# Kernel optimization log

Measured on AMD Instinct MI355X. Metric: run time of the kernel, lower is better.

## Reference

```python
import jax, jax.numpy as jnp
import numpy as np

B, N, D, F = 32, 96, 32, 16


def setup_inputs() -> dict:
    key = jax.random.key(0)
    ks = jax.random.split(key, 10)
    s = 0.1
    nodes = jax.random.normal(ks[0], (B, N, D), dtype=jnp.float32)
    edges = jax.random.normal(ks[1], (B, N * N, F), dtype=jnp.float32)
    mask = (jax.random.uniform(ks[2], (B, N * N, 1)) < 0.3).astype(jnp.float32)
    # GRU_Aggregator: Linear(F -> D*D) + ReLU
    W_agg = jax.random.normal(ks[3], (F, D * D), dtype=jnp.float32) * s
    b_agg = jax.random.normal(ks[4], (D * D,), dtype=jnp.float32) * s
    # GRU_Combiner: nn.GRU(input_size=D, hidden_size=D), gate order r,z,n
    w_ih = jax.random.normal(ks[5], (3 * D, D), dtype=jnp.float32) * s
    w_hh = jax.random.normal(ks[6], (3 * D, D), dtype=jnp.float32) * s
    b_ih = jax.random.normal(ks[7], (3 * D,), dtype=jnp.float32) * s
    b_hh = jax.random.normal(ks[8], (3 * D,), dtype=jnp.float32) * s
    return {"nodes": nodes, "edges": edges, "mask": mask,
            "W_agg": W_agg, "b_agg": b_agg,
            "w_ih": w_ih, "w_hh": w_hh, "b_ih": b_ih, "b_hh": b_hh}


def _gru_cell(h, x, w_ih, w_hh, b_ih, b_hh):
    # torch nn.GRU cell: gates in (r, z, n) order
    gi = x @ w_ih.T + b_ih  # [..., 3D]
    gh = h @ w_hh.T + b_hh
    i_r, i_z, i_n = jnp.split(gi, 3, axis=-1)
    h_r, h_z, h_n = jnp.split(gh, 3, axis=-1)
    r = jax.nn.sigmoid(i_r + h_r)
    z = jax.nn.sigmoid(i_z + h_z)
    n = jnp.tanh(i_n + r * h_n)
    return (1.0 - z) * n + z * h


def reference(nodes, edges, mask, W_agg, b_agg, w_ih, w_hh, b_ih, b_hh):
    b, n, d = nodes.shape
    # edge-conditioned per-edge matrices A: [B, N*N, D, D]
    A = jax.nn.relu(edges @ W_agg + b_agg).reshape(b, n * n, d, d)
    # state_j = nodes.repeat(1, N, 1): entry (i*N + j) is nodes[:, j]
    state_j = jnp.tile(nodes, (1, n, 1))  # [B, N*N, D]
    messages = jnp.einsum('bepq,beq->bep', A, state_j)  # [B, N*N, D]
    masked = (messages * mask).reshape(b, n, n, d)
    agg_m = masked.sum(axis=2)  # [B, N, D]
    # GRU combiner: sequence [old_state, agg_messages], h0 = 0, take last output
    h = jnp.zeros((b, n, d), dtype=nodes.dtype)
    h = _gru_cell(h, nodes, w_ih, w_hh, b_ih, b_hh)
    h = _gru_cell(h, agg_m, w_ih, w_hh, b_ih, b_hh)
    return h
```

## Files before the change

kernel.cpp:

```cpp
#include <hip/hip_runtime.h>
#include <math.h>

#define BB 32
#define NN 96
#define DD 32
#define FF 16
#define NE (NN * NN)
#define PAIRS (BB * NN)
#define PPB 6
#define GRID_F (PAIRS / PPB)
#define EG 6

__device__ __forceinline__ float dot32(const float* __restrict__ x,
                                       const float* __restrict__ w) {
    float s = 0.f;
    #pragma unroll
    for (int u = 0; u < 8; ++u) {
        float4 a = *(const float4*)(x + 4 * u);
        float4 c = *(const float4*)(w + 4 * u);
        s = fmaf(a.x, c.x, fmaf(a.y, c.y, fmaf(a.z, c.z, fmaf(a.w, c.w, s))));
    }
    return s;
}
__device__ __forceinline__ float sigm(float x) { return 1.f / (1.f + expf(-x)); }

__global__ __launch_bounds__(512, 2)
void mp_fused(const float* __restrict__ nodes, const float* __restrict__ edges,
              const float* __restrict__ mask, const float* __restrict__ W_agg,
              const float* __restrict__ b_agg,
              const float* __restrict__ w_ih, const float* __restrict__ w_hh,
              const float* __restrict__ b_ih, const float* __restrict__ b_hh,
              float* __restrict__ out) {
    __shared__ __align__(16) float Wl[FF * 1024];
    __shared__ __align__(16) float nodl[NN * DD];
    __shared__ int jlist[2][NN];
    __shared__ int jcnt[2];
    __shared__ __align__(16) float aggv[PPB][DD];
    __shared__ __align__(16) float h1v[PPB][DD];
    __shared__ float bih_s[96], bhh_s[96];

    const int tid  = threadIdx.x;
    const int lane = tid & 63;
    const int wv   = tid >> 6;
    const int tq   = wv & 3;
    const int psel = wv >> 2;
    const int pair0 = blockIdx.x * PPB;
    const int b  = pair0 / NN;
    const int i0 = pair0 % NN;
    const int l8 = lane & 7;
    const int lp = lane >> 3;
    const int wbase = 256 * tq + 4 * lane;

    for (int v = tid; v < 4096; v += 512)
        ((float4*)Wl)[v] = ((const float4*)W_agg)[v];
    for (int v = tid; v < 768; v += 512)
        ((float4*)nodl)[v] = ((const float4*)(nodes + b * NN * DD))[v];

    const float4 bvv = *(const float4*)(b_agg + wbase);

    for (int pr = 0; pr < 3; ++pr) {
        __syncthreads();
        if (tid < 2) jcnt[tid] = 0;
        __syncthreads();
        if (tid < 2 * NN) {
            const int ps = tid / NN, col = tid % NN;
            const int ii = i0 + 2 * pr + ps;
            if (mask[(size_t)b * NE + (size_t)ii * NN + col] != 0.f) {
                int p = atomicAdd(&jcnt[ps], 1);
                jlist[ps][p] = col;
            }
        }
        __syncthreads();
        const int i = i0 + 2 * pr + psel;
        const int cnt = __builtin_amdgcn_readfirstlane(jcnt[psel]);
        const float4* ebase4 =
            (const float4*)(edges + ((size_t)b * NE + (size_t)i * NN) * FF);

        float aggacc = 0.f;
        for (int e0 = 0; e0 < cnt; e0 += EG) {
            int jj[EG];
            #pragma unroll
            for (int e = 0; e < EG; ++e) {
                int idx = e0 + e; if (idx > cnt - 1) idx = cnt - 1;
                jj[e] = __builtin_amdgcn_readfirstlane(jlist[psel][idx]);
            }
            float acc[EG][4];
            #pragma unroll
            for (int e = 0; e < EG; ++e) {
                acc[e][0] = bvv.x; acc[e][1] = bvv.y;
                acc[e][2] = bvv.z; acc[e][3] = bvv.w;
            }
            #pragma unroll
            for (int u = 0; u < 4; ++u) {
                float4 ev[EG];
                #pragma unroll
                for (int e = 0; e < EG; ++e) ev[e] = ebase4[jj[e] * 4 + u];
                #pragma unroll
                for (int f2 = 0; f2 < 4; ++f2) {
                    const float4 w4 =
                        *(const float4*)(Wl + (4 * u + f2) * 1024 + wbase);
                    #pragma unroll
                    for (int e = 0; e < EG; ++e) {
                        const float ef = (f2 == 0) ? ev[e].x : (f2 == 1) ? ev[e].y
                                       : (f2 == 2) ? ev[e].z : ev[e].w;
                        acc[e][0] = fmaf(ef, w4.x, acc[e][0]);
                        acc[e][1] = fmaf(ef, w4.y, acc[e][1]);
                        acc[e][2] = fmaf(ef, w4.z, acc[e][2]);
                        acc[e][3] = fmaf(ef, w4.w, acc[e][3]);
                    }
                }
            }
            #pragma unroll
            for (int e = 0; e < EG; ++e) {
                if (e0 + e < cnt) {
                    const float4 x4 =
                        *(const float4*)(nodl + jj[e] * DD + 4 * l8);
                    aggacc = fmaf(fmaxf(acc[e][0], 0.f), x4.x, aggacc);
                    aggacc = fmaf(fmaxf(acc[e][1], 0.f), x4.y, aggacc);
                    aggacc = fmaf(fmaxf(acc[e][2], 0.f), x4.z, aggacc);
                    aggacc = fmaf(fmaxf(acc[e][3], 0.f), x4.w, aggacc);
                }
            }
        }
        aggacc += __shfl_xor(aggacc, 1, 64);
        aggacc += __shfl_xor(aggacc, 2, 64);
        aggacc += __shfl_xor(aggacc, 4, 64);
        if (l8 == 0) aggv[2 * pr + psel][8 * tq + lp] = aggacc;
    }

    __syncthreads();
    float* wihL = Wl;
    float* whhL = Wl + 3456;
    for (int v = tid; v < 768; v += 512) {
        int row = v >> 3, c4 = v & 7;
        *(float4*)&wihL[row * 36 + c4 * 4] = ((const float4*)w_ih)[v];
        *(float4*)&whhL[row * 36 + c4 * 4] = ((const float4*)w_hh)[v];
    }
    if (tid < 96) { bih_s[tid] = b_ih[tid]; bhh_s[tid] = b_hh[tid]; }
    __syncthreads();

    if (tid < PPB * DD) {
        const int pp = tid >> 5, d = tid & 31;
        const float* x = nodl + (i0 + pp) * DD;
        float gi_r = dot32(x, &wihL[(0 * 32 + d) * 36]) + bih_s[d];
        float gi_z = dot32(x, &wihL[(1 * 32 + d) * 36]) + bih_s[32 + d];
        float gi_n = dot32(x, &wihL[(2 * 32 + d) * 36]) + bih_s[64 + d];
        float r1 = sigm(gi_r + bhh_s[d]);
        float z1 = sigm(gi_z + bhh_s[32 + d]);
        float n1 = tanhf(gi_n + r1 * bhh_s[64 + d]);
        h1v[pp][d] = (1.f - z1) * n1;
    }
    __syncthreads();
    if (tid < PPB * DD) {
        const int pp = tid >> 5, d = tid & 31;
        const float* a  = &aggv[pp][0];
        const float* h1 = &h1v[pp][0];
        float gi_r = dot32(a, &wihL[(0 * 32 + d) * 36]) + bih_s[d];
        float gi_z = dot32(a, &wihL[(1 * 32 + d) * 36]) + bih_s[32 + d];
        float gi_n = dot32(a, &wihL[(2 * 32 + d) * 36]) + bih_s[64 + d];
        float gh_r = dot32(h1, &whhL[(0 * 32 + d) * 36]) + bhh_s[d];
        float gh_z = dot32(h1, &whhL[(1 * 32 + d) * 36]) + bhh_s[32 + d];
        float gh_n = dot32(h1, &whhL[(2 * 32 + d) * 36]) + bhh_s[64 + d];
        float r2 = sigm(gi_r + gh_r);
        float z2 = sigm(gi_z + gh_z);
        float n2 = tanhf(gi_n + r2 * gh_n);
        float h2 = (1.f - z2) * n2 + z2 * h1[d];
        out[(size_t)(pair0 + pp) * DD + d] = h2;
    }
}

extern "C" void kernel_launch(void* const* d_in, const int* in_sizes, int n_in,
                              void* d_out, int out_size, void* d_ws, size_t ws_size,
                              hipStream_t stream) {
    const float* nodes = (const float*)d_in[0];
    const float* edges = (const float*)d_in[1];
    const float* mask  = (const float*)d_in[2];
    const float* W_agg = (const float*)d_in[3];
    const float* b_agg = (const float*)d_in[4];
    const float* w_ih  = (const float*)d_in[5];
    const float* w_hh  = (const float*)d_in[6];
    const float* b_ih  = (const float*)d_in[7];
    const float* b_hh  = (const float*)d_in[8];
    float* out = (float*)d_out;

    mp_fused<<<GRID_F, 512, 0, stream>>>(nodes, edges, mask, W_agg, b_agg,
                                         w_ih, w_hh, b_ih, b_hh, out);
}
```

Baseline: 158.0 us.

## Gather masked edges into LDS and load-balance edge groups across waves

Doubles the rows per block to 12 and the block size to 1024 threads. All masked edge rows for those 12 rows are gathered into shared memory in one coalesced pass before any compute starts. Work is then split into a flat list of six-edge groups that the four wave slots take in turn, with partial results merged through shared-memory atomics. This replaces the old per-row-pair sequential passes and their barriers, and it spreads uneven mask counts across waves. The cost is more shared memory, at most one block per CU, and half as many blocks in the grid.

After: 311.9 us. 97.5% more time.

```diff
diff --git a/kernel.cpp b/kernel.cpp
--- a/kernel.cpp
+++ b/kernel.cpp
@@ -7,9 +7,10 @@
 #define FF 16
 #define NE (NN * NN)
 #define PAIRS (BB * NN)
-#define PPB 6
+#define PPB 12
 #define GRID_F (PAIRS / PPB)
 #define EG 6
+#define MAXG (PPB * 16)
 
 __device__ __forceinline__ float dot32(const float* __restrict__ x,
                                        const float* __restrict__ w) {
@@ -24,7 +25,7 @@
 }
 __device__ __forceinline__ float sigm(float x) { return 1.f / (1.f + expf(-x)); }
 
-__global__ __launch_bounds__(512, 2)
+__global__ __launch_bounds__(1024)
 void mp_fused(const float* __restrict__ nodes, const float* __restrict__ edges,
               const float* __restrict__ mask, const float* __restrict__ W_agg,
               const float* __restrict__ b_agg,
@@ -33,17 +34,21 @@
               float* __restrict__ out) {
     __shared__ __align__(16) float Wl[FF * 1024];
     __shared__ __align__(16) float nodl[NN * DD];
-    __shared__ int jlist[2][NN];
-    __shared__ int jcnt[2];
-    __shared__ __align__(16) float aggv[PPB][DD];
-    __shared__ __align__(16) float h1v[PPB][DD];
+    __shared__ float4 ebufq[PPB * 384];
+    __shared__ int   jlf[PPB * NN];
+    __shared__ int   jcnt[PPB];
+    __shared__ int   g2p[MAXG];
+    __shared__ int   g2e0[MAXG];
+    __shared__ int   gtot_s;
+    __shared__ float aggv[PPB][DD];
+    __shared__ float h1v[PPB][DD];
     __shared__ float bih_s[96], bhh_s[96];
 
     const int tid  = threadIdx.x;
     const int lane = tid & 63;
     const int wv   = tid >> 6;
     const int tq   = wv & 3;
-    const int psel = wv >> 2;
+    const int s    = wv >> 2;
     const int pair0 = blockIdx.x * PPB;
     const int b  = pair0 / NN;
     const int i0 = pair0 % NN;
@@ -51,90 +56,124 @@
     const int lp = lane >> 3;
     const int wbase = 256 * tq + 4 * lane;
 
-    for (int v = tid; v < 4096; v += 512)
-        ((float4*)Wl)[v] = ((const float4*)W_agg)[v];
-    for (int v = tid; v < 768; v += 512)
-        ((float4*)nodl)[v] = ((const float4*)(nodes + b * NN * DD))[v];
-
+    if (tid < PPB) jcnt[tid] = 0;
+    if (tid < PPB * DD) ((float*)aggv)[tid] = 0.f;
+    #pragma unroll
+    for (int c = 0; c < 4; ++c)
+        ((float4*)Wl)[c * 1024 + tid] = ((const float4*)W_agg)[c * 1024 + tid];
+    if (tid < 768)
+        ((float4*)nodl)[tid] = ((const float4*)(nodes + b * NN * DD))[tid];
     const float4 bvv = *(const float4*)(b_agg + wbase);
-
-    for (int pr = 0; pr < 3; ++pr) {
-        __syncthreads();
-        if (tid < 2) jcnt[tid] = 0;
-        __syncthreads();
-        if (tid < 2 * NN) {
-            const int ps = tid / NN, col = tid % NN;
-            const int ii = i0 + 2 * pr + ps;
-            if (mask[(size_t)b * NE + (size_t)ii * NN + col] != 0.f) {
-                int p = atomicAdd(&jcnt[ps], 1);
-                jlist[ps][p] = col;
-            }
-        }
-        __syncthreads();
-        const int i = i0 + 2 * pr + psel;
-        const int cnt = __builtin_amdgcn_readfirstlane(jcnt[psel]);
-        const float4* ebase4 =
-            (const float4*)(edges + ((size_t)b * NE + (size_t)i * NN) * FF);
-
-        float aggacc = 0.f;
-        for (int e0 = 0; e0 < cnt; e0 += EG) {
-            int jj[EG];
+    __syncthreads();
+
+    for (int v = tid; v < PPB * NN; v += 1024) {
+        const int p = v / NN, col = v % NN;
+        if (mask[(size_t)b * NE + (size_t)(i0 + p) * NN + col] != 0.f) {
+            int pos = atomicAdd(&jcnt[p], 1);
+            jlf[p * NN + pos] = col;
+        }
+    }
+    __syncthreads();
+
+    if (tid < PPB) {
+        int gs = 0;
+        for (int q = 0; q < PPB; ++q)
+            if (q < tid) gs += (jcnt[q] + EG - 1) / EG;
+        const int gp = (jcnt[tid] + EG - 1) / EG;
+        for (int g = 0; g < gp; ++g) { g2p[gs + g] = tid; g2e0[gs + g] = g * EG; }
+        if (tid == PPB - 1) gtot_s = gs + gp;
+    }
+    {
+        float4 sv[5];
+        bool   sa[5];
+        #pragma unroll
+        for (int k = 0; k < 5; ++k) {
+            const int t = tid + k * 1024;
+            bool act = (t < PPB * 384);
+            int p = 0, e = 0, ch = 0;
+            if (act) {
+                p = t / 384; const int lt = t - p * 384;
+                e = lt >> 2; ch = lt & 3;
+                act = (e < jcnt[p]);
+            }
+            sa[k] = act;
+            if (act) {
+                const int row = jlf[p * NN + e];
+                sv[k] = *(const float4*)(edges +
+                    ((size_t)b * NE + (size_t)(i0 + p) * NN + row) * FF + ch * 4);
+            }
+        }
+        #pragma unroll
+        for (int k = 0; k < 5; ++k)
+            if (sa[k]) ebufq[tid + k * 1024] = sv[k];
+    }
+    __syncthreads();
+
+    const float4* Wlq   = (const float4*)Wl;
+    const float4* nodlq = (const float4*)nodl;
+    const int Gtot = gtot_s;
+    const int wq4  = 64 * tq + lane;
+    for (int fg = s; fg < Gtot; fg += 4) {
+        const int p   = __builtin_amdgcn_readfirstlane(g2p[fg]);
+        const int e0g = __builtin_amdgcn_readfirstlane(g2e0[fg]);
+        const int cnt = __builtin_amdgcn_readfirstlane(jcnt[p]);
+        const int ecnt = cnt - e0g;
+        int jj[EG];
+        #pragma unroll
+        for (int e = 0; e < EG; ++e) {
+            int idx = e0g + e; if (idx > cnt - 1) idx = cnt - 1;
+            jj[e] = __builtin_amdgcn_readfirstlane(jlf[p * NN + idx]);
+        }
+        float acc[EG][4];
+        #pragma unroll
+        for (int e = 0; e < EG; ++e) {
+            acc[e][0] = bvv.x; acc[e][1] = bvv.y;
+            acc[e][2] = bvv.z; acc[e][3] = bvv.w;
+        }
+        const float4* fb = ebufq + p * 384 + e0g * 4;
+        #pragma unroll
+        for (int u = 0; u < 4; ++u) {
+            float4 ev[EG];
             #pragma unroll
-            for (int e = 0; e < EG; ++e) {
-                int idx = e0 + e; if (idx > cnt - 1) idx = cnt - 1;
-                jj[e] = __builtin_amdgcn_readfirstlane(jlist[psel][idx]);
-            }
-            float acc[EG][4];
+            for (int e = 0; e < EG; ++e) ev[e] = fb[e * 4 + u];
             #pragma unroll
-            for (int e = 0; e < EG; ++e) {
-                acc[e][0] = bvv.x; acc[e][1] = bvv.y;
-                acc[e][2] = bvv.z; acc[e][3] = bvv.w;
-            }
-            #pragma unroll
-            for (int u = 0; u < 4; ++u) {
-                float4 ev[EG];
+            for (int f2 = 0; f2 < 4; ++f2) {
+                const float4 w4 = Wlq[(4 * u + f2) * 256 + wq4];
                 #pragma unroll
-                for (int e = 0; e < EG; ++e) ev[e] = ebase4[jj[e] * 4 + u];
-                #pragma unroll
-                for (int f2 = 0; f2 < 4; ++f2) {
-                    const float4 w4 =
-                        *(const float4*)(Wl + (4 * u + f2) * 1024 + wbase);
-                    #pragma unroll
-                    for (int e = 0; e < EG; ++e) {
-                        const float ef = (f2 == 0) ? ev[e].x : (f2 == 1) ? ev[e].y
-                                       : (f2 == 2) ? ev[e].z : ev[e].w;
-                        acc[e][0] = fmaf(ef, w4.x, acc[e][0]);
-                        acc[e][1] = fmaf(ef, w4.y, acc[e][1]);
-                        acc[e][2] = fmaf(ef, w4.z, acc[e][2]);
-                        acc[e][3] = fmaf(ef, w4.w, acc[e][3]);
-                    }
+                for (int e = 0; e < EG; ++e) {
+                    const float ef = (f2 == 0) ? ev[e].x : (f2 == 1) ? ev[e].y
+                                   : (f2 == 2) ? ev[e].z : ev[e].w;
+                    acc[e][0] = fmaf(ef, w4.x, acc[e][0]);
+                    acc[e][1] = fmaf(ef, w4.y, acc[e][1]);
+                    acc[e][2] = fmaf(ef, w4.z, acc[e][2]);
+                    acc[e][3] = fmaf(ef, w4.w, acc[e][3]);
                 }
             }
-            #pragma unroll
-            for (int e = 0; e < EG; ++e) {
-                if (e0 + e < cnt) {
-                    const float4 x4 =
-                        *(const float4*)(nodl + jj[e] * DD + 4 * l8);
-                    aggacc = fmaf(fmaxf(acc[e][0], 0.f), x4.x, aggacc);
-                    aggacc = fmaf(fmaxf(acc[e][1], 0.f), x4.y, aggacc);
-                    aggacc = fmaf(fmaxf(acc[e][2], 0.f), x4.z, aggacc);
-                    aggacc = fmaf(fmaxf(acc[e][3], 0.f), x4.w, aggacc);
-                }
-            }
-        }
-        aggacc += __shfl_xor(aggacc, 1, 64);
-        aggacc += __shfl_xor(aggacc, 2, 64);
-        aggacc += __shfl_xor(aggacc, 4, 64);
-        if (l8 == 0) aggv[2 * pr + psel][8 * tq + lp] = aggacc;
-    }
-
-    __syncthreads();
+        }
+        float r = 0.f;
+        #pragma unroll
+        for (int e = 0; e < EG; ++e) {
+            if (e < ecnt) {
+                const float4 x4 = nodlq[jj[e] * 8 + l8];
+                r = fmaf(fmaxf(acc[e][0], 0.f), x4.x, r);
+                r = fmaf(fmaxf(acc[e][1], 0.f), x4.y, r);
+                r = fmaf(fmaxf(acc[e][2], 0.f), x4.z, r);
+                r = fmaf(fmaxf(acc[e][3], 0.f), x4.w, r);
+            }
+        }
+        r += __shfl_xor(r, 1, 64);
+        r += __shfl_xor(r, 2, 64);
+        r += __shfl_xor(r, 4, 64);
+        if (l8 == 0) atomicAdd(&aggv[p][8 * tq + lp], r);
+    }
+    __syncthreads();
+
     float* wihL = Wl;
     float* whhL = Wl + 3456;
-    for (int v = tid; v < 768; v += 512) {
-        int row = v >> 3, c4 = v & 7;
-        *(float4*)&wihL[row * 36 + c4 * 4] = ((const float4*)w_ih)[v];
-        *(float4*)&whhL[row * 36 + c4 * 4] = ((const float4*)w_hh)[v];
+    if (tid < 768) {
+        const int row = tid >> 3, c4 = tid & 7;
+        *(float4*)&wihL[row * 36 + c4 * 4] = ((const float4*)w_ih)[tid];
+        *(float4*)&whhL[row * 36 + c4 * 4] = ((const float4*)w_hh)[tid];
     }
     if (tid < 96) { bih_s[tid] = b_ih[tid]; bhh_s[tid] = b_hh[tid]; }
     __syncthreads();
@@ -183,6 +222,6 @@
     const float* b_hh  = (const float*)d_in[8];
     float* out = (float*)d_out;
 
-    mp_fused<<<GRID_F, 512, 0, stream>>>(nodes, edges, mask, W_agg, b_agg,
-                                         w_ih, w_hh, b_ih, b_hh, out);
+    mp_fused<<<GRID_F, 1024, 0, stream>>>(nodes, edges, mask, W_agg, b_agg,
+                                          w_ih, w_hh, b_ih, b_hh, out);
 }
```
